# Kernel tuning notes

Measured on AMD Instinct MI355X. Metric: run time of the kernel, lower is better.

## Reference

```python
import jax, jax.numpy as jnp
import numpy as np

D_MODEL, NHEAD, D_K = 512, 8, 64
MIN_RBF, MAX_RBF = 0.1, 0.9
MIN_SPREAD, MAX_SPREAD, BASE = 1.0, 6.0, 20.0
LN_EPS = 1e-5


def _layernorm(x, w, b):
    mu = jnp.mean(x, axis=-1, keepdims=True)
    var = jnp.var(x, axis=-1, keepdims=True)
    return (x - mu) * jax.lax.rsqrt(var + LN_EPS) * w + b


def setup_inputs() -> dict:
    key = jax.random.key(0)
    ks = jax.random.split(key, 10)
    B, N = 1, 2048
    inp = {
        "q": jax.random.normal(ks[0], (B, N, D_MODEL), jnp.float32),
        "k": jax.random.normal(ks[1], (B, N, D_MODEL), jnp.float32),
        "v": jax.random.normal(ks[2], (B, N, D_MODEL), jnp.float32),
        "coords": jax.random.normal(ks[3], (B, N, 3), jnp.float32) * 3.0,
        "key_padding_mask": jnp.zeros((B, N), bool),
        # learned params (torch.randn init for projections, LN defaults)
        "q_proj": jax.random.normal(ks[4], (NHEAD, D_MODEL, D_K), jnp.float32),
        "k_proj": jax.random.normal(ks[5], (NHEAD, D_MODEL, D_K), jnp.float32),
        "v_proj": jax.random.normal(ks[6], (NHEAD, D_MODEL, D_K), jnp.float32),
        "q_ln_w": jnp.ones((D_K,), jnp.float32), "q_ln_b": jnp.zeros((D_K,), jnp.float32),
        "k_ln_w": jnp.ones((D_K,), jnp.float32), "k_ln_b": jnp.zeros((D_K,), jnp.float32),
        "v_ln_w": jnp.ones((D_K,), jnp.float32), "v_ln_b": jnp.zeros((D_K,), jnp.float32),
        "out_w": jax.random.normal(ks[7], (D_MODEL, D_MODEL), jnp.float32) / np.sqrt(D_MODEL),
        "out_b": jnp.zeros((D_MODEL,), jnp.float32),
    }
    return inp


def reference(q, k, v, coords, key_padding_mask,
              q_proj, k_proj, v_proj,
              q_ln_w, q_ln_b, k_ln_w, k_ln_b, v_ln_w, v_ln_b,
              out_w, out_b):
    B, N, _ = q.shape
    # per-head projections: [B,H,N,dk]
    Q = _layernorm(jnp.einsum('bnd,hdk->bhnk', q, q_proj), q_ln_w, q_ln_b)
    K = _layernorm(jnp.einsum('bnd,hdk->bhnk', k, k_proj), k_ln_w, k_ln_b)
    V = _layernorm(jnp.einsum('bnd,hdk->bhnk', v, v_proj), v_ln_w, v_ln_b)

    # head-specific gaussian spreads (torch.logspace(0,1,H,base) semantics)
    spreads = MIN_SPREAD + (MAX_SPREAD - MIN_SPREAD) * (BASE ** jnp.linspace(0.0, 1.0, NHEAD) - 1.0) / (BASE - 1.0)

    # pairwise squared distances [B,N,N] -> per-head RBF [B,H,N,N]
    d2 = jnp.sum((coords[:, :, None, :] - coords[:, None, :, :]) ** 2, axis=-1)
    rbf = jnp.exp(-d2[:, None, :, :] / (2.0 * spreads[None, :, None, None] ** 2))
    rbf = jnp.clip(rbf, MIN_RBF, MAX_RBF)

    # RBF-modulated scaled dot-product attention
    scores = jnp.einsum('bhik,bhjk->bhij', Q, K) / np.sqrt(D_K) * rbf
    scores = jnp.where(key_padding_mask[:, None, None, :], -1e9, scores)
    P = jax.nn.softmax(scores, axis=-1)
    out = jnp.einsum('bhij,bhjk->bhik', P, V)  # [B,H,N,dk]

    # torch: out.permute(0,2,3,1).reshape(B,N,d_model)
    out = jnp.transpose(out, (0, 2, 3, 1)).reshape(B, N, D_MODEL)
    return out @ out_w.T + out_b
```

## Files before the change

kernel.cpp:

```cpp
#include <hip/hip_runtime.h>
#include <math.h>

#define N_TOK 2048
#define D_MODEL 512
#define NHEAD 8
#define DK 64
#define LOG2E 1.44269504f
#define QSCALE 0.18033688f
#define KTILE 6144
#define KHEAD (32 * KTILE)

typedef __attribute__((ext_vector_type(8))) short short8;
typedef __attribute__((ext_vector_type(4))) short short4v;
typedef __attribute__((ext_vector_type(4))) float f32x4;

__device__ __forceinline__ short f2bf(float x) {
    unsigned u = __float_as_uint(x);
    u = (u + 0x7fffu + ((u >> 16) & 1u)) >> 16;
    return (short)u;
}

__device__ __forceinline__ float bf2f(short s) {
    return __uint_as_float(((unsigned)(unsigned short)s) << 16);
}

__device__ __forceinline__ void split2(float x, short& h_, short& l_) {
    h_ = f2bf(x);
    l_ = f2bf(x - bf2f(h_));
}

__device__ __forceinline__ void split3(float x, short& h_, short& m_, short& l_) {
    h_ = f2bf(x);
    float r = x - bf2f(h_);
    m_ = f2bf(r);
    l_ = f2bf(r - bf2f(m_));
}

__device__ __forceinline__ unsigned cvt_pk_bf16(float lo, float hi) {
    unsigned r;
    asm("v_cvt_pk_bf16_f32 %0, %1, %2" : "=v"(r) : "v"(lo), "v"(hi));
    return r;
}

__device__ __forceinline__ float head_c(int h) {
    float tt = (float)h * (1.0f / 7.0f);
    float sp = 1.0f + 5.0f * (__builtin_exp2f(tt * 4.3219281f) - 1.0f) * (1.0f / 19.0f);
    return -LOG2E / (2.0f * sp * sp);
}

__global__ __launch_bounds__(256) void prep_all_kernel(
    const float* __restrict__ q, const float* __restrict__ k,
    const float* __restrict__ v, const float* __restrict__ coords,
    const unsigned char* __restrict__ mask,
    const float* __restrict__ qp, const float* __restrict__ kp,
    const float* __restrict__ vp, const float* __restrict__ ow,
    short* __restrict__ Xbf, short* __restrict__ Wt, short* __restrict__ Wo,
    short* __restrict__ Kf, float* __restrict__ mpen,
    unsigned* __restrict__ tflag)
{
    __shared__ float tile[64][65];
    const int bid = blockIdx.x;
    const int t = threadIdx.x;

    if (bid < 1536) {
        int i = bid * 256 + t;
        int tt = i >> 17;
        int rem = i & 131071;
        const float4* src = (const float4*)(tt == 0 ? q : (tt == 1 ? k : v));
        float4 a = src[rem * 2], b = src[rem * 2 + 1];
        short8 o;
        o[0] = f2bf(a.x); o[1] = f2bf(a.y); o[2] = f2bf(a.z); o[3] = f2bf(a.w);
        o[4] = f2bf(b.x); o[5] = f2bf(b.y); o[6] = f2bf(b.z); o[7] = f2bf(b.w);
        *(short8*)(Xbf + (size_t)i * 8) = o;
    } else if (bid < 1792) {
        int i = bid - 1536;
        int z = i >> 6;
        int bx = i & 7, by = (i >> 3) & 7;
        if (z == 3) {
            int m0 = bx * 64, j0 = by * 64, hh = by;
            for (int ii = t; ii < 4096; ii += 256) {
                int r = ii >> 6, kk = ii & 63;
                Wo[(size_t)(m0 + r) * 512 + j0 + kk] =
                    f2bf(ow[(size_t)(m0 + r) * 512 + kk * 8 + hh]);
            }
            return;
        }
        const float* src = z == 0 ? qp : (z == 1 ? kp : vp);
        const int h = bx, d0 = by * 64;
        for (int ii = t; ii < 4096; ii += 256) {
            int r = ii >> 6, c = ii & 63;
            tile[r][c] = src[((size_t)h * 512 + d0 + r) * 64 + c];
        }
        __syncthreads();
        short* W = Wt + (size_t)z * 512 * 512;
        for (int ii = t; ii < 4096; ii += 256) {
            int cr = ii >> 6, dc_ = ii & 63;
            W[(size_t)(h * 64 + cr) * 512 + d0 + dc_] = f2bf(tile[dc_][cr]);
        }
    } else {
        int j = (bid - 1792) * 256 + t;
        float x = coords[j * 3 + 0], y = coords[j * 3 + 1], z = coords[j * 3 + 2];
        unsigned char mk = mask[j];
        mpen[j] = mk ? -1e9f : 0.f;
        unsigned long long b = __ballot(mk != 0);
        if ((t & 63) == 0) tflag[j >> 6] = (b != 0ull) ? 1u : 0u;
        float n2 = x * x + y * y + z * z;
        const short one = (short)0x3F80;
        const int kr = j & 15;
        #pragma unroll
        for (int h = 0; h < NHEAD; ++h) {
            float c = head_c(h);
            short ahx, alx, ahy, aly, ahz, alz, k2a, k2b, k2c;
            split2(-2.f * c * x, ahx, alx);
            split2(-2.f * c * y, ahy, aly);
            split2(-2.f * c * z, ahz, alz);
            split3(c * n2, k2a, k2b, k2c);
            short8 g0, g1, g2;
            g0[0] = ahx; g0[1] = alx; g0[2] = ahx; g0[3] = ahy;
            g0[4] = aly; g0[5] = ahy; g0[6] = ahz; g0[7] = alz;
            g1[0] = ahz; g1[1] = alx; g1[2] = aly; g1[3] = alz;
            g1[4] = k2a; g1[5] = k2b; g1[6] = k2c; g1[7] = one;
            g2[0] = one; g2[1] = one;
            #pragma unroll
            for (int e = 2; e < 8; ++e) g2[e] = 0;
            short8 g3;
            #pragma unroll
            for (int e = 0; e < 8; ++e) g3[e] = 0;
            short* base = Kf + (size_t)h * KHEAD + (size_t)(j >> 6) * KTILE
                        + 4096 + (size_t)((j >> 4) & 3) * 512;
            *(short8*)(base + (size_t)(0 * 16 + kr) * 8) = g0;
            *(short8*)(base + (size_t)(1 * 16 + kr) * 8) = g1;
            *(short8*)(base + (size_t)(2 * 16 + kr) * 8) = g2;
            *(short8*)(base + (size_t)(3 * 16 + kr) * 8) = g3;
        }
    }
}

__global__ __launch_bounds__(256) void proj_ln_mfma_kernel(
    const short* __restrict__ Xbf, const short* __restrict__ Wt,
    const float* __restrict__ qlw, const float* __restrict__ qlb,
    const float* __restrict__ klw, const float* __restrict__ klb,
    const float* __restrict__ vlw, const float* __restrict__ vlb,
    short* __restrict__ Qbf, short* __restrict__ Kf, short* __restrict__ Vf)
{
    __shared__ short Xs[64 * 64];
    __shared__ short Ws[64 * 64];
    const int z = blockIdx.z, h = blockIdx.y;
    const int n0 = blockIdx.x * 64;
    const int tid = threadIdx.x, w = tid >> 6, l = tid & 63;
    const int l15 = l & 15, lg = l >> 4;

    const short* X = Xbf + (size_t)z * N_TOK * D_MODEL;
    const short* Wz = Wt + ((size_t)z * 512 + h * 64) * 512;

    const f32x4 zero4 = {0.f, 0.f, 0.f, 0.f};
    f32x4 acc[4];
    #pragma unroll
    for (int dc = 0; dc < 4; ++dc) acc[dc] = zero4;

    for (int kb = 0; kb < 8; ++kb) {
        const int d0 = kb * 64;
        __syncthreads();
        #pragma unroll
        for (int i = 0; i < 2; ++i) {
            int c = tid + i * 256;
            int r = c >> 3, g = c & 7;
            short8 xv = *(const short8*)(X + (size_t)(n0 + r) * 512 + d0 + g * 8);
            *(short8*)(Xs + r * 64 + ((g * 8) ^ ((r & 7) << 3))) = xv;
            short8 wv = *(const short8*)(Wz + (size_t)r * 512 + d0 + g * 8);
            *(short8*)(Ws + r * 64 + ((g * 8) ^ ((r & 7) << 3))) = wv;
        }
        __syncthreads();
        const int arow = w * 16 + l15;
        short8 a0 = *(const short8*)(Xs + arow * 64 + ((lg * 8) ^ ((arow & 7) << 3)));
        short8 a1 = *(const short8*)(Xs + arow * 64 + ((32 + lg * 8) ^ ((arow & 7) << 3)));
        #pragma unroll
        for (int dc = 0; dc < 4; ++dc) {
            const int brow = dc * 16 + l15;
            short8 b0 = *(const short8*)(Ws + brow * 64 + ((lg * 8) ^ ((brow & 7) << 3)));
            acc[dc] = __builtin_amdgcn_mfma_f32_16x16x32_bf16(a0, b0, acc[dc], 0, 0, 0);
            short8 b1 = *(const short8*)(Ws + brow * 64 + ((32 + lg * 8) ^ ((brow & 7) << 3)));
            acc[dc] = __builtin_amdgcn_mfma_f32_16x16x32_bf16(a1, b1, acc[dc], 0, 0, 0);
        }
    }

    const float* lw  = z == 0 ? qlw : (z == 1 ? klw : vlw);
    const float* lbp = z == 0 ? qlb : (z == 1 ? klb : vlb);
    float wv_[4], bv_[4];
    #pragma unroll
    for (int dc = 0; dc < 4; ++dc) {
        wv_[dc] = lw[dc * 16 + l15];
        bv_[dc] = lbp[dc * 16 + l15];
    }
    float mu[4], rs[4];
    #pragma unroll
    for (int reg = 0; reg < 4; ++reg) {
        float s = acc[0][reg] + acc[1][reg] + acc[2][reg] + acc[3][reg];
        #pragma unroll
        for (int off = 1; off < 16; off <<= 1) s += __shfl_xor(s, off);
        float m = s * (1.0f / 64.0f);
        float ss = 0.f;
        #pragma unroll
        for (int dc = 0; dc < 4; ++dc) { float d = acc[dc][reg] - m; ss += d * d; }
        #pragma unroll
        for (int off = 1; off < 16; off <<= 1) ss += __shfl_xor(ss, off);
        mu[reg] = m;
        rs[reg] = rsqrtf(ss * (1.0f / 64.0f) + 1e-5f);
    }

    const int tile = n0 >> 6;
    if (z == 0) {
        #pragma unroll
        for (int dc = 0; dc < 4; ++dc)
            #pragma unroll
            for (int reg = 0; reg < 4; ++reg) {
                int n = n0 + w * 16 + lg * 4 + reg;
                float val = ((acc[dc][reg] - mu[reg]) * rs[reg] * wv_[dc] + bv_[dc]) * QSCALE;
                Qbf[((size_t)h * N_TOK + n) * DK + dc * 16 + l15] = f2bf(val);
            }
    } else if (z == 1) {
        short* Kh = Kf + (size_t)h * KHEAD;
        #pragma unroll
        for (int dc = 0; dc < 4; ++dc) {
            int hf  = dc >> 1;
            int lgc = ((dc & 1) << 1) | (l15 >> 3);
            int e   = l15 & 7;
            size_t base = (size_t)tile * KTILE + (w * 2 + hf) * 512 + 16 * 8 * lgc + e;
            #pragma unroll
            for (int reg = 0; reg < 4; ++reg) {
                float val = (acc[dc][reg] - mu[reg]) * rs[reg] * wv_[dc] + bv_[dc];
                Kh[base + (lg * 4 + reg) * 8] = f2bf(val);
            }
        }
    } else {
        short* Vh = Vf + (size_t)h * N_TOK * DK;
        int hfv = w >> 1;
        int lgv = ((w & 1) << 1) | (lg >> 1);
        int eb  = (lg & 1) * 4;
        #pragma unroll
        for (int dc = 0; dc < 4; ++dc) {
            short4v p;
            #pragma unroll
            for (int reg = 0; reg < 4; ++reg)
                p[reg] = f2bf((acc[dc][reg] - mu[reg]) * rs[reg] * wv_[dc] + bv_[dc]);
            size_t addr = (size_t)tile * 4096 + (dc * 2 + hfv) * 512 + (l15 + 16 * lgv) * 8 + eb;
            *(short4v*)(Vh + addr) = p;
        }
    }
}

__global__ __launch_bounds__(256) void attn_kernel(
    const short* __restrict__ Qbf, const short* __restrict__ Kf,
    const short* __restrict__ Vf, const float* __restrict__ coords,
    const float* __restrict__ mpen, const unsigned* __restrict__ tflag,
    short* __restrict__ PO, float* __restrict__ PL)
{
    __shared__ short Pls[4][1024];
    __shared__ float bufO[2][64][17];
    __shared__ float bufL[2][64];

    const int tid = threadIdx.x;
    const int w = tid >> 6, l = tid & 63;
    const int l15 = l & 15, lg = l >> 4;
    const int bid = blockIdx.x;
    const int h  = bid & 7;
    const int nt = (bid >> 3) & 127;
    const int z  = bid >> 10;
    const int n0 = nt * 16;

    char* Pb = (char*)&Pls[w][0];
    const int psw = (l15 & 7) << 4;

    const short* Qrow = Qbf + ((size_t)h * N_TOK + n0 + l15) * DK + lg * 8;
    const short8 qf0 = *(const short8*)(Qrow);
    const short8 qf1 = *(const short8*)(Qrow + 32);

    const float ch = head_c(h);
    const float qx = coords[(n0 + l15) * 3 + 0];
    const float qy = coords[(n0 + l15) * 3 + 1];
    const float qz = coords[(n0 + l15) * 3 + 2];
    const float cq2 = ch * (qx * qx + qy * qy + qz * qz);
    short8 qaug;
    {
        const short one = (short)0x3F80;
        short qhx, qlx, qhy, qly, qhz, qlz, q2a, q2b, q2c;
        split2(qx, qhx, qlx);
        split2(qy, qhy, qly);
        split2(qz, qhz, qlz);
        split3(cq2, q2a, q2b, q2c);
        #pragma unroll
        for (int e = 0; e < 8; ++e) qaug[e] = 0;
        if (lg == 0) {
            qaug[0] = qhx; qaug[1] = qhx; qaug[2] = qlx; qaug[3] = qhy;
            qaug[4] = qhy; qaug[5] = qly; qaug[6] = qhz; qaug[7] = qhz;
        } else if (lg == 1) {
            qaug[0] = qlz; qaug[1] = qlx; qaug[2] = qly; qaug[3] = qlz;
            qaug[4] = one; qaug[5] = one; qaug[6] = one; qaug[7] = q2a;
        } else if (lg == 2) {
            qaug[0] = q2b; qaug[1] = q2c;
        }
    }

    short8 ones8;
    #pragma unroll
    for (int i = 0; i < 8; ++i) ones8[i] = (short)0x3F80;

    const f32x4 zero4 = {0.f, 0.f, 0.f, 0.f};
    f32x4 oacc[4];
    f32x4 oacc_l = zero4;
    #pragma unroll
    for (int i = 0; i < 4; ++i) oacc[i] = zero4;

    const short* Kfh = Kf + (size_t)h * KHEAD;
    const short* Vfh = Vf + (size_t)h * N_TOK * DK;

    for (int t = 0; t < 4; ++t) {
        const int kt = (z * 4 + w) * 4 + t;
        const int kbase = kt * 64;
        const short* kp = Kfh + (size_t)kt * KTILE + l * 8;
        const short* ap = Kfh + (size_t)kt * KTILE + 4096 + l * 8;
        const short* vp = Vfh + (size_t)kt * 4096 + l * 8;

        f32x4 sacc[4], aacc[4];
        #pragma unroll
        for (int nc = 0; nc < 4; ++nc) {
            short8 k0 = *(const short8*)(kp + nc * 1024);
            short8 k1 = *(const short8*)(kp + nc * 1024 + 512);
            short8 ka = *(const short8*)(ap + nc * 512);
            sacc[nc] = __builtin_amdgcn_mfma_f32_16x16x32_bf16(k0, qf0, zero4, 0, 0, 0);
            sacc[nc] = __builtin_amdgcn_mfma_f32_16x16x32_bf16(k1, qf1, sacc[nc], 0, 0, 0);
            aacc[nc] = __builtin_amdgcn_mfma_f32_16x16x32_bf16(ka, qaug, zero4, 0, 0, 0);
        }

        #pragma unroll
        for (int nc = 0; nc < 4; ++nc) {
            #pragma unroll
            for (int reg = 0; reg < 4; ++reg) {
                float rb = __builtin_exp2f(aacc[nc][reg]);
                rb = fminf(fmaxf(rb, 0.1f), 0.9f);
                sacc[nc][reg] *= rb;
            }
        }
        if (tflag[kt]) {
            #pragma unroll
            for (int nc = 0; nc < 4; ++nc)
                #pragma unroll
                for (int reg = 0; reg < 4; ++reg)
                    sacc[nc][reg] += mpen[kbase + nc * 16 + lg * 4 + reg];
        }

        #pragma unroll
        for (int nc = 0; nc < 4; ++nc) {
            float p0 = __builtin_exp2f(sacc[nc][0]);
            float p1 = __builtin_exp2f(sacc[nc][1]);
            float p2 = __builtin_exp2f(sacc[nc][2]);
            float p3 = __builtin_exp2f(sacc[nc][3]);
            uint2 u;
            u.x = cvt_pk_bf16(p0, p1);
            u.y = cvt_pk_bf16(p2, p3);
            *(uint2*)(Pb + ((l15 * 128 + nc * 32 + lg * 8) ^ psw)) = u;
        }

        short8 pf0 = *(const short8*)(Pb + ((l15 * 128 + lg * 16) ^ psw));
        short8 pf1 = *(const short8*)(Pb + ((l15 * 128 + 64 + lg * 16) ^ psw));
        #pragma unroll
        for (int dcc = 0; dcc < 4; ++dcc) {
            short8 v0 = *(const short8*)(vp + dcc * 1024);
            short8 v1 = *(const short8*)(vp + dcc * 1024 + 512);
            oacc[dcc] = __builtin_amdgcn_mfma_f32_16x16x32_bf16(v0, pf0, oacc[dcc], 0, 0, 0);
            oacc[dcc] = __builtin_amdgcn_mfma_f32_16x16x32_bf16(v1, pf1, oacc[dcc], 0, 0, 0);
        }
        oacc_l = __builtin_amdgcn_mfma_f32_16x16x32_bf16(ones8, pf0, oacc_l, 0, 0, 0);
        oacc_l = __builtin_amdgcn_mfma_f32_16x16x32_bf16(ones8, pf1, oacc_l, 0, 0, 0);
    }

    float l_ = oacc_l[0];

    if (w >= 2) {
        int slot = w - 2;
        bufL[slot][l] = l_;
        #pragma unroll
        for (int dc = 0; dc < 4; ++dc)
            #pragma unroll
            for (int reg = 0; reg < 4; ++reg)
                bufO[slot][l][dc * 4 + reg] = oacc[dc][reg];
    }
    __syncthreads();
    if (w < 2) {
        l_ += bufL[w][l];
        #pragma unroll
        for (int dc = 0; dc < 4; ++dc)
            #pragma unroll
            for (int reg = 0; reg < 4; ++reg)
                oacc[dc][reg] += bufO[w][l][dc * 4 + reg];
    }
    __syncthreads();
    if (w == 1) {
        bufL[0][l] = l_;
        #pragma unroll
        for (int dc = 0; dc < 4; ++dc)
            #pragma unroll
            for (int reg = 0; reg < 4; ++reg)
                bufO[0][l][dc * 4 + reg] = oacc[dc][reg];
    }
    __syncthreads();
    if (w == 0) {
        float lf = l_ + bufL[0][l];
        size_t p = ((size_t)z * NHEAD + h) * N_TOK + n0 + l15;
        if (lg == 0) PL[p] = lf;
        #pragma unroll
        for (int dcc = 0; dcc < 4; ++dcc) {
            short4v o4;
            #pragma unroll
            for (int reg = 0; reg < 4; ++reg)
                o4[reg] = f2bf(oacc[dcc][reg] + bufO[0][l][dcc * 4 + reg]);
            *(short4v*)(PO + p * 64 + dcc * 16 + lg * 4) = o4;
        }
    }
}

__global__ __launch_bounds__(256) void out_proj_kernel(
    const short* __restrict__ PO, const float* __restrict__ PL,
    const short* __restrict__ Wo, const float* __restrict__ bias,
    float* __restrict__ out)
{
    __shared__ short As[64 * 64];
    __shared__ short Bs[64 * 64];
    const int n0 = blockIdx.x * 64, m0 = blockIdx.y * 64;
    const int tid = threadIdx.x, w = tid >> 6, l = tid & 63;
    const int l15 = l & 15, lg = l >> 4;

    const f32x4 zero4 = {0.f, 0.f, 0.f, 0.f};
    f32x4 acc[4];
    #pragma unroll
    for (int dc = 0; dc < 4; ++dc) acc[dc] = zero4;

    for (int kb = 0; kb < 8; ++kb) {
        const int j0 = kb * 64;
        __syncthreads();
        #pragma unroll
        for (int i = 0; i < 2; ++i) {
            int c = tid + i * 256;
            int r = c >> 3, g = c & 7;
            int n = n0 + r;
            size_t p0 = (size_t)kb * N_TOK + n;
            size_t p1 = (size_t)(NHEAD + kb) * N_TOK + n;
            float rl = 1.0f / (PL[p0] + PL[p1]);
            short8 a0 = *(const short8*)(PO + p0 * 64 + g * 8);
            short8 a1 = *(const short8*)(PO + p1 * 64 + g * 8);
            short8 av;
            #pragma unroll
            for (int e = 0; e < 8; ++e)
                av[e] = f2bf((bf2f(a0[e]) + bf2f(a1[e])) * rl);
            *(short8*)(As + r * 64 + ((g * 8) ^ ((r & 7) << 3))) = av;
            short8 bv = *(const short8*)(Wo + (size_t)(m0 + r) * 512 + j0 + g * 8);
            *(short8*)(Bs + r * 64 + ((g * 8) ^ ((r & 7) << 3))) = bv;
        }
        __syncthreads();
        const int arow = w * 16 + l15;
        short8 a0 = *(const short8*)(As + arow * 64 + ((lg * 8) ^ ((arow & 7) << 3)));
        short8 a1 = *(const short8*)(As + arow * 64 + ((32 + lg * 8) ^ ((arow & 7) << 3)));
        #pragma unroll
        for (int dc = 0; dc < 4; ++dc) {
            const int brow = dc * 16 + l15;
            short8 b0 = *(const short8*)(Bs + brow * 64 + ((lg * 8) ^ ((brow & 7) << 3)));
            acc[dc] = __builtin_amdgcn_mfma_f32_16x16x32_bf16(a0, b0, acc[dc], 0, 0, 0);
            short8 b1 = *(const short8*)(Bs + brow * 64 + ((32 + lg * 8) ^ ((brow & 7) << 3)));
            acc[dc] = __builtin_amdgcn_mfma_f32_16x16x32_bf16(a1, b1, acc[dc], 0, 0, 0);
        }
    }

    #pragma unroll
    for (int dc = 0; dc < 4; ++dc) {
        float bm = bias[m0 + dc * 16 + l15];
        #pragma unroll
        for (int reg = 0; reg < 4; ++reg) {
            int n = n0 + w * 16 + lg * 4 + reg;
            out[(size_t)n * D_MODEL + m0 + dc * 16 + l15] = acc[dc][reg] + bm;
        }
    }
}

extern "C" void kernel_launch(void* const* d_in, const int* in_sizes, int n_in,
                              void* d_out, int out_size, void* d_ws, size_t ws_size,
                              hipStream_t stream)
{
    const float* q      = (const float*)d_in[0];
    const float* k      = (const float*)d_in[1];
    const float* v      = (const float*)d_in[2];
    const float* coords = (const float*)d_in[3];
    const unsigned char* mask = (const unsigned char*)d_in[4];
    const float* q_proj = (const float*)d_in[5];
    const float* k_proj = (const float*)d_in[6];
    const float* v_proj = (const float*)d_in[7];
    const float* q_ln_w = (const float*)d_in[8];
    const float* q_ln_b = (const float*)d_in[9];
    const float* k_ln_w = (const float*)d_in[10];
    const float* k_ln_b = (const float*)d_in[11];
    const float* v_ln_w = (const float*)d_in[12];
    const float* v_ln_b = (const float*)d_in[13];
    const float* out_w  = (const float*)d_in[14];
    const float* out_b  = (const float*)d_in[15];
    float* out = (float*)d_out;

    short* Xbf = (short*)d_ws;
    short* Wt  = Xbf + 3145728;
    short* Wo  = Wt + 786432;
    short* Qbf = Wo + 262144;
    short* Kf  = Qbf + 1048576;
    short* Vf  = Kf + 1572864;
    float* mpen = (float*)(Vf + 1048576);
    unsigned* tflag = (unsigned*)(mpen + 2048);

    short* PO = Xbf;
    float* PL = (float*)Wt;

    prep_all_kernel<<<dim3(1800), dim3(256), 0, stream>>>(
        q, k, v, coords, mask, q_proj, k_proj, v_proj, out_w,
        Xbf, Wt, Wo, Kf, mpen, tflag);
    proj_ln_mfma_kernel<<<dim3(32, 8, 3), dim3(256), 0, stream>>>(
        Xbf, Wt, q_ln_w, q_ln_b, k_ln_w, k_ln_b, v_ln_w, v_ln_b, Qbf, Kf, Vf);
    attn_kernel<<<dim3(2048), dim3(256), 0, stream>>>(
        Qbf, Kf, Vf, coords, mpen, tflag, PO, PL);
    out_proj_kernel<<<dim3(32, 8), dim3(256), 0, stream>>>(PO, PL, Wo, out_b, out);
}
```

Baseline: 66.85 us.

## Process two 16-query tiles per attention block to reuse K/V fragment loads

Each attention block now handles 32 query rows (two 16-row halves) instead of 16, so each K, augmented-coordinate and V fragment loaded from global memory feeds twice as many MFMAs. The grid is halved to 1024 blocks and the LDS staging and cross-wave reduction buffers are doubled to match. This cuts global/L2 traffic for K and V per query but doubles accumulator registers per thread, which may lower occupancy. A launch-bounds hint of three blocks per CU is added.

Measured after the change: 68.29 us. 2.1% more time.

```diff
diff --git a/kernel.cpp b/kernel.cpp
--- a/kernel.cpp
+++ b/kernel.cpp
@@ -249,67 +249,75 @@
     }
 }
 
-__global__ __launch_bounds__(256) void attn_kernel(
+__global__ __launch_bounds__(256, 3) void attn_kernel(
     const short* __restrict__ Qbf, const short* __restrict__ Kf,
     const short* __restrict__ Vf, const float* __restrict__ coords,
     const float* __restrict__ mpen, const unsigned* __restrict__ tflag,
     short* __restrict__ PO, float* __restrict__ PL)
 {
-    __shared__ short Pls[4][1024];
-    __shared__ float bufO[2][64][17];
-    __shared__ float bufL[2][64];
+    __shared__ short Pls[4][2048];
+    __shared__ float bufO[2][64][33];
+    __shared__ float bufL[2][64][2];
 
     const int tid = threadIdx.x;
     const int w = tid >> 6, l = tid & 63;
     const int l15 = l & 15, lg = l >> 4;
     const int bid = blockIdx.x;
     const int h  = bid & 7;
-    const int nt = (bid >> 3) & 127;
-    const int z  = bid >> 10;
-    const int n0 = nt * 16;
-
-    char* Pb = (char*)&Pls[w][0];
+    const int nt = (bid >> 3) & 63;
+    const int z  = bid >> 9;
+    const int n0 = nt * 32;
+
+    char* PbA = (char*)&Pls[w][0];
+    char* PbB = (char*)&Pls[w][1024];
     const int psw = (l15 & 7) << 4;
 
-    const short* Qrow = Qbf + ((size_t)h * N_TOK + n0 + l15) * DK + lg * 8;
-    const short8 qf0 = *(const short8*)(Qrow);
-    const short8 qf1 = *(const short8*)(Qrow + 32);
+    const short* QrowA = Qbf + ((size_t)h * N_TOK + n0 + l15) * DK + lg * 8;
+    const short8 qfA0 = *(const short8*)(QrowA);
+    const short8 qfA1 = *(const short8*)(QrowA + 32);
+    const short* QrowB = QrowA + 16 * DK;
+    const short8 qfB0 = *(const short8*)(QrowB);
+    const short8 qfB1 = *(const short8*)(QrowB + 32);
 
     const float ch = head_c(h);
-    const float qx = coords[(n0 + l15) * 3 + 0];
-    const float qy = coords[(n0 + l15) * 3 + 1];
-    const float qz = coords[(n0 + l15) * 3 + 2];
-    const float cq2 = ch * (qx * qx + qy * qy + qz * qz);
-    short8 qaug;
-    {
-        const short one = (short)0x3F80;
+    const short one = (short)0x3F80;
+    short8 qaugA, qaugB;
+    #pragma unroll
+    for (int half = 0; half < 2; ++half) {
+        int n = n0 + half * 16 + l15;
+        float qx = coords[n * 3 + 0];
+        float qy = coords[n * 3 + 1];
+        float qz = coords[n * 3 + 2];
+        float cq2 = ch * (qx * qx + qy * qy + qz * qz);
         short qhx, qlx, qhy, qly, qhz, qlz, q2a, q2b, q2c;
         split2(qx, qhx, qlx);
         split2(qy, qhy, qly);
         split2(qz, qhz, qlz);
         split3(cq2, q2a, q2b, q2c);
-        #pragma unroll
-        for (int e = 0; e < 8; ++e) qaug[e] = 0;
+        short8 qa;
+        #pragma unroll
+        for (int e = 0; e < 8; ++e) qa[e] = 0;
         if (lg == 0) {
-            qaug[0] = qhx; qaug[1] = qhx; qaug[2] = qlx; qaug[3] = qhy;
-            qaug[4] = qhy; qaug[5] = qly; qaug[6] = qhz; qaug[7] = qhz;
+            qa[0] = qhx; qa[1] = qhx; qa[2] = qlx; qa[3] = qhy;
+            qa[4] = qhy; qa[5] = qly; qa[6] = qhz; qa[7] = qhz;
         } else if (lg == 1) {
-            qaug[0] = qlz; qaug[1] = qlx; qaug[2] = qly; qaug[3] = qlz;
-            qaug[4] = one; qaug[5] = one; qaug[6] = one; qaug[7] = q2a;
+            qa[0] = qlz; qa[1] = qlx; qa[2] = qly; qa[3] = qlz;
+            qa[4] = one; qa[5] = one; qa[6] = one; qa[7] = q2a;
         } else if (lg == 2) {
-            qaug[0] = q2b; qaug[1] = q2c;
-        }
+            qa[0] = q2b; qa[1] = q2c;
+        }
+        if (half == 0) qaugA = qa; else qaugB = qa;
     }
 
     short8 ones8;
     #pragma unroll
-    for (int i = 0; i < 8; ++i) ones8[i] = (short)0x3F80;
+    for (int i = 0; i < 8; ++i) ones8[i] = one;
 
     const f32x4 zero4 = {0.f, 0.f, 0.f, 0.f};
-    f32x4 oacc[4];
-    f32x4 oacc_l = zero4;
-    #pragma unroll
-    for (int i = 0; i < 4; ++i) oacc[i] = zero4;
+    f32x4 oaccA[4], oaccB[4];
+    f32x4 olA = zero4, olB = zero4;
+    #pragma unroll
+    for (int i = 0; i < 4; ++i) { oaccA[i] = zero4; oaccB[i] = zero4; }
 
     const short* Kfh = Kf + (size_t)h * KHEAD;
     const short* Vfh = Vf + (size_t)h * N_TOK * DK;
@@ -318,103 +326,131 @@
         const int kt = (z * 4 + w) * 4 + t;
         const int kbase = kt * 64;
         const short* kp = Kfh + (size_t)kt * KTILE + l * 8;
-        const short* ap = Kfh + (size_t)kt * KTILE + 4096 + l * 8;
+        const short* ap = kp + 4096;
         const short* vp = Vfh + (size_t)kt * 4096 + l * 8;
 
-        f32x4 sacc[4], aacc[4];
+        f32x4 sA[4], sB[4], aA[4], aB[4];
         #pragma unroll
         for (int nc = 0; nc < 4; ++nc) {
             short8 k0 = *(const short8*)(kp + nc * 1024);
             short8 k1 = *(const short8*)(kp + nc * 1024 + 512);
             short8 ka = *(const short8*)(ap + nc * 512);
-            sacc[nc] = __builtin_amdgcn_mfma_f32_16x16x32_bf16(k0, qf0, zero4, 0, 0, 0);
-            sacc[nc] = __builtin_amdgcn_mfma_f32_16x16x32_bf16(k1, qf1, sacc[nc], 0, 0, 0);
-            aacc[nc] = __builtin_amdgcn_mfma_f32_16x16x32_bf16(ka, qaug, zero4, 0, 0, 0);
+            sA[nc] = __builtin_amdgcn_mfma_f32_16x16x32_bf16(k0, qfA0, zero4, 0, 0, 0);
+            sA[nc] = __builtin_amdgcn_mfma_f32_16x16x32_bf16(k1, qfA1, sA[nc], 0, 0, 0);
+            sB[nc] = __builtin_amdgcn_mfma_f32_16x16x32_bf16(k0, qfB0, zero4, 0, 0, 0);
+            sB[nc] = __builtin_amdgcn_mfma_f32_16x16x32_bf16(k1, qfB1, sB[nc], 0, 0, 0);
+            aA[nc] = __builtin_amdgcn_mfma_f32_16x16x32_bf16(ka, qaugA, zero4, 0, 0, 0);
+            aB[nc] = __builtin_amdgcn_mfma_f32_16x16x32_bf16(ka, qaugB, zero4, 0, 0, 0);
         }
 
         #pragma unroll
         for (int nc = 0; nc < 4; ++nc) {
             #pragma unroll
             for (int reg = 0; reg < 4; ++reg) {
-                float rb = __builtin_exp2f(aacc[nc][reg]);
-                rb = fminf(fmaxf(rb, 0.1f), 0.9f);
-                sacc[nc][reg] *= rb;
+                float rbA = __builtin_exp2f(aA[nc][reg]);
+                rbA = fminf(fmaxf(rbA, 0.1f), 0.9f);
+                sA[nc][reg] *= rbA;
+                float rbB = __builtin_exp2f(aB[nc][reg]);
+                rbB = fminf(fmaxf(rbB, 0.1f), 0.9f);
+                sB[nc][reg] *= rbB;
             }
         }
         if (tflag[kt]) {
             #pragma unroll
             for (int nc = 0; nc < 4; ++nc)
                 #pragma unroll
-                for (int reg = 0; reg < 4; ++reg)
-                    sacc[nc][reg] += mpen[kbase + nc * 16 + lg * 4 + reg];
+                for (int reg = 0; reg < 4; ++reg) {
+                    float mp = mpen[kbase + nc * 16 + lg * 4 + reg];
+                    sA[nc][reg] += mp;
+                    sB[nc][reg] += mp;
+                }
         }
 
         #pragma unroll
         for (int nc = 0; nc < 4; ++nc) {
-            float p0 = __builtin_exp2f(sacc[nc][0]);
-            float p1 = __builtin_exp2f(sacc[nc][1]);
-            float p2 = __builtin_exp2f(sacc[nc][2]);
-            float p3 = __builtin_exp2f(sacc[nc][3]);
-            uint2 u;
-            u.x = cvt_pk_bf16(p0, p1);
-            u.y = cvt_pk_bf16(p2, p3);
-            *(uint2*)(Pb + ((l15 * 128 + nc * 32 + lg * 8) ^ psw)) = u;
-        }
-
-        short8 pf0 = *(const short8*)(Pb + ((l15 * 128 + lg * 16) ^ psw));
-        short8 pf1 = *(const short8*)(Pb + ((l15 * 128 + 64 + lg * 16) ^ psw));
+            uint2 uA, uB;
+            uA.x = cvt_pk_bf16(__builtin_exp2f(sA[nc][0]), __builtin_exp2f(sA[nc][1]));
+            uA.y = cvt_pk_bf16(__builtin_exp2f(sA[nc][2]), __builtin_exp2f(sA[nc][3]));
+            uB.x = cvt_pk_bf16(__builtin_exp2f(sB[nc][0]), __builtin_exp2f(sB[nc][1]));
+            uB.y = cvt_pk_bf16(__builtin_exp2f(sB[nc][2]), __builtin_exp2f(sB[nc][3]));
+            *(uint2*)(PbA + ((l15 * 128 + nc * 32 + lg * 8) ^ psw)) = uA;
+            *(uint2*)(PbB + ((l15 * 128 + nc * 32 + lg * 8) ^ psw)) = uB;
+        }
+
+        short8 pfA0 = *(const short8*)(PbA + ((l15 * 128 + lg * 16) ^ psw));
+        short8 pfA1 = *(const short8*)(PbA + ((l15 * 128 + 64 + lg * 16) ^ psw));
+        short8 pfB0 = *(const short8*)(PbB + ((l15 * 128 + lg * 16) ^ psw));
+        short8 pfB1 = *(const short8*)(PbB + ((l15 * 128 + 64 + lg * 16) ^ psw));
         #pragma unroll
         for (int dcc = 0; dcc < 4; ++dcc) {
             short8 v0 = *(const short8*)(vp + dcc * 1024);
             short8 v1 = *(const short8*)(vp + dcc * 1024 + 512);
-            oacc[dcc] = __builtin_amdgcn_mfma_f32_16x16x32_bf16(v0, pf0, oacc[dcc], 0, 0, 0);
-            oacc[dcc] = __builtin_amdgcn_mfma_f32_16x16x32_bf16(v1, pf1, oacc[dcc], 0, 0, 0);
-        }
-        oacc_l = __builtin_amdgcn_mfma_f32_16x16x32_bf16(ones8, pf0, oacc_l, 0, 0, 0);
-        oacc_l = __builtin_amdgcn_mfma_f32_16x16x32_bf16(ones8, pf1, oacc_l, 0, 0, 0);
-    }
-
-    float l_ = oacc_l[0];
+            oaccA[dcc] = __builtin_amdgcn_mfma_f32_16x16x32_bf16(v0, pfA0, oaccA[dcc], 0, 0, 0);
+            oaccA[dcc] = __builtin_amdgcn_mfma_f32_16x16x32_bf16(v1, pfA1, oaccA[dcc], 0, 0, 0);
+            oaccB[dcc] = __builtin_amdgcn_mfma_f32_16x16x32_bf16(v0, pfB0, oaccB[dcc], 0, 0, 0);
+            oaccB[dcc] = __builtin_amdgcn_mfma_f32_16x16x32_bf16(v1, pfB1, oaccB[dcc], 0, 0, 0);
+        }
+        olA = __builtin_amdgcn_mfma_f32_16x16x32_bf16(ones8, pfA0, olA, 0, 0, 0);
+        olA = __builtin_amdgcn_mfma_f32_16x16x32_bf16(ones8, pfA1, olA, 0, 0, 0);
+        olB = __builtin_amdgcn_mfma_f32_16x16x32_bf16(ones8, pfB0, olB, 0, 0, 0);
+        olB = __builtin_amdgcn_mfma_f32_16x16x32_bf16(ones8, pfB1, olB, 0, 0, 0);
+    }
+
+    float lA = olA[0], lB = olB[0];
 
     if (w >= 2) {
         int slot = w - 2;
-        bufL[slot][l] = l_;
+        bufL[slot][l][0] = lA;
+        bufL[slot][l][1] = lB;
         #pragma unroll
         for (int dc = 0; dc < 4; ++dc)
             #pragma unroll
-            for (int reg = 0; reg < 4; ++reg)
-                bufO[slot][l][dc * 4 + reg] = oacc[dc][reg];
+            for (int reg = 0; reg < 4; ++reg) {
+                bufO[slot][l][dc * 4 + reg] = oaccA[dc][reg];
+                bufO[slot][l][16 + dc * 4 + reg] = oaccB[dc][reg];
+            }
     }
     __syncthreads();
     if (w < 2) {
-        l_ += bufL[w][l];
+        lA += bufL[w][l][0];
+        lB += bufL[w][l][1];
         #pragma unroll
         for (int dc = 0; dc < 4; ++dc)
             #pragma unroll
-            for (int reg = 0; reg < 4; ++reg)
-                oacc[dc][reg] += bufO[w][l][dc * 4 + reg];
+            for (int reg = 0; reg < 4; ++reg) {
+                oaccA[dc][reg] += bufO[w][l][dc * 4 + reg];
+                oaccB[dc][reg] += bufO[w][l][16 + dc * 4 + reg];
+            }
     }
     __syncthreads();
     if (w == 1) {
-        bufL[0][l] = l_;
+        bufL[0][l][0] = lA;
+        bufL[0][l][1] = lB;
         #pragma unroll
         for (int dc = 0; dc < 4; ++dc)
             #pragma unroll
-            for (int reg = 0; reg < 4; ++reg)
-                bufO[0][l][dc * 4 + reg] = oacc[dc][reg];
+            for (int reg = 0; reg < 4; ++reg) {
+                bufO[0][l][dc * 4 + reg] = oaccA[dc][reg];
+                bufO[0][l][16 + dc * 4 + reg] = oaccB[dc][reg];
+            }
     }
     __syncthreads();
     if (w == 0) {
-        float lf = l_ + bufL[0][l];
-        size_t p = ((size_t)z * NHEAD + h) * N_TOK + n0 + l15;
-        if (lg == 0) PL[p] = lf;
+        float lfA = lA + bufL[0][l][0];
+        float lfB = lB + bufL[0][l][1];
+        size_t pA = ((size_t)z * NHEAD + h) * N_TOK + n0 + l15;
+        size_t pB = pA + 16;
+        if (lg == 0) { PL[pA] = lfA; PL[pB] = lfB; }
         #pragma unroll
         for (int dcc = 0; dcc < 4; ++dcc) {
-            short4v o4;
-            #pragma unroll
-            for (int reg = 0; reg < 4; ++reg)
-                o4[reg] = f2bf(oacc[dcc][reg] + bufO[0][l][dcc * 4 + reg]);
-            *(short4v*)(PO + p * 64 + dcc * 16 + lg * 4) = o4;
+            short4v oA, oB;
+            #pragma unroll
+            for (int reg = 0; reg < 4; ++reg) {
+                oA[reg] = f2bf(oaccA[dcc][reg] + bufO[0][l][dcc * 4 + reg]);
+                oB[reg] = f2bf(oaccB[dcc][reg] + bufO[0][l][16 + dcc * 4 + reg]);
+            }
+            *(short4v*)(PO + pA * 64 + dcc * 16 + lg * 4) = oA;
+            *(short4v*)(PO + pB * 64 + dcc * 16 + lg * 4) = oB;
         }
     }
 }
@@ -520,7 +556,7 @@
         Xbf, Wt, Wo, Kf, mpen, tflag);
     proj_ln_mfma_kernel<<<dim3(32, 8, 3), dim3(256), 0, stream>>>(
         Xbf, Wt, q_ln_w, q_ln_b, k_ln_w, k_ln_b, v_ln_w, v_ln_b, Qbf, Kf, Vf);
-    attn_kernel<<<dim3(2048), dim3(256), 0, stream>>>(
+    attn_kernel<<<dim3(1024), dim3(256), 0, stream>>>(
         Qbf, Kf, Vf, coords, mpen, tflag, PO, PL);
     out_proj_kernel<<<dim3(32, 8), dim3(256), 0, stream>>>(PO, PL, Wo, out_b, out);
 }
```

## Fuse fp32-to-bf16 input conversion into projection GEMM and double row tile

Applied to the files above, without the earlier changes.

Drops the separate pass in the prep kernel that wrote bf16 copies of q/k/v. The projection kernel now reads fp32 inputs directly and converts them while staging into shared memory. Each block also covers 128 tokens instead of 64, so every loaded weight tile feeds twice as many MFMAs and the grid shrinks to 384 blocks. The workspace layout is reshuffled to match. The trade-off is that each projection block reads twice the bytes per input element (fp32) and has fewer blocks to spread across CUs.

Result: no change. 67.88 us (+1.5%).

```diff
diff --git a/kernel.cpp b/kernel.cpp
--- a/kernel.cpp
+++ b/kernel.cpp
@@ -49,12 +49,10 @@
 }
 
 __global__ __launch_bounds__(256) void prep_all_kernel(
-    const float* __restrict__ q, const float* __restrict__ k,
-    const float* __restrict__ v, const float* __restrict__ coords,
-    const unsigned char* __restrict__ mask,
+    const float* __restrict__ coords, const unsigned char* __restrict__ mask,
     const float* __restrict__ qp, const float* __restrict__ kp,
     const float* __restrict__ vp, const float* __restrict__ ow,
-    short* __restrict__ Xbf, short* __restrict__ Wt, short* __restrict__ Wo,
+    short* __restrict__ Wt, short* __restrict__ Wo,
     short* __restrict__ Kf, float* __restrict__ mpen,
     unsigned* __restrict__ tflag)
 {
@@ -62,18 +60,8 @@
     const int bid = blockIdx.x;
     const int t = threadIdx.x;
 
-    if (bid < 1536) {
-        int i = bid * 256 + t;
-        int tt = i >> 17;
-        int rem = i & 131071;
-        const float4* src = (const float4*)(tt == 0 ? q : (tt == 1 ? k : v));
-        float4 a = src[rem * 2], b = src[rem * 2 + 1];
-        short8 o;
-        o[0] = f2bf(a.x); o[1] = f2bf(a.y); o[2] = f2bf(a.z); o[3] = f2bf(a.w);
-        o[4] = f2bf(b.x); o[5] = f2bf(b.y); o[6] = f2bf(b.z); o[7] = f2bf(b.w);
-        *(short8*)(Xbf + (size_t)i * 8) = o;
-    } else if (bid < 1792) {
-        int i = bid - 1536;
+    if (bid < 256) {
+        int i = bid;
         int z = i >> 6;
         int bx = i & 7, by = (i >> 3) & 7;
         if (z == 3) {
@@ -98,7 +86,7 @@
             W[(size_t)(h * 64 + cr) * 512 + d0 + dc_] = f2bf(tile[dc_][cr]);
         }
     } else {
-        int j = (bid - 1792) * 256 + t;
+        int j = (bid - 256) * 256 + t;
         float x = coords[j * 3 + 0], y = coords[j * 3 + 1], z = coords[j * 3 + 2];
         unsigned char mk = mask[j];
         mpen[j] = mk ? -1e9f : 0.f;
@@ -137,50 +125,68 @@
 }
 
 __global__ __launch_bounds__(256) void proj_ln_mfma_kernel(
-    const short* __restrict__ Xbf, const short* __restrict__ Wt,
+    const float* __restrict__ xq, const float* __restrict__ xk,
+    const float* __restrict__ xv, const short* __restrict__ Wt,
     const float* __restrict__ qlw, const float* __restrict__ qlb,
     const float* __restrict__ klw, const float* __restrict__ klb,
     const float* __restrict__ vlw, const float* __restrict__ vlb,
     short* __restrict__ Qbf, short* __restrict__ Kf, short* __restrict__ Vf)
 {
-    __shared__ short Xs[64 * 64];
+    __shared__ short Xs[128 * 64];
     __shared__ short Ws[64 * 64];
     const int z = blockIdx.z, h = blockIdx.y;
-    const int n0 = blockIdx.x * 64;
+    const int n0 = blockIdx.x * 128;
     const int tid = threadIdx.x, w = tid >> 6, l = tid & 63;
     const int l15 = l & 15, lg = l >> 4;
 
-    const short* X = Xbf + (size_t)z * N_TOK * D_MODEL;
+    const float* X = z == 0 ? xq : (z == 1 ? xk : xv);
     const short* Wz = Wt + ((size_t)z * 512 + h * 64) * 512;
 
     const f32x4 zero4 = {0.f, 0.f, 0.f, 0.f};
-    f32x4 acc[4];
-    #pragma unroll
-    for (int dc = 0; dc < 4; ++dc) acc[dc] = zero4;
+    f32x4 acc[2][4];
+    #pragma unroll
+    for (int H = 0; H < 2; ++H)
+        #pragma unroll
+        for (int dc = 0; dc < 4; ++dc) acc[H][dc] = zero4;
 
     for (int kb = 0; kb < 8; ++kb) {
         const int d0 = kb * 64;
         __syncthreads();
         #pragma unroll
+        for (int i = 0; i < 8; ++i) {
+            int idx = tid + i * 256;
+            int r = idx >> 4;
+            int f = idx & 15;
+            float4 xv4 = *(const float4*)(X + (size_t)(n0 + r) * 512 + d0 + f * 4);
+            short4v pk;
+            pk[0] = f2bf(xv4.x); pk[1] = f2bf(xv4.y);
+            pk[2] = f2bf(xv4.z); pk[3] = f2bf(xv4.w);
+            *(short4v*)(Xs + r * 64 + (((f >> 1) * 8) ^ ((r & 7) << 3)) + (f & 1) * 4) = pk;
+        }
+        #pragma unroll
         for (int i = 0; i < 2; ++i) {
             int c = tid + i * 256;
             int r = c >> 3, g = c & 7;
-            short8 xv = *(const short8*)(X + (size_t)(n0 + r) * 512 + d0 + g * 8);
-            *(short8*)(Xs + r * 64 + ((g * 8) ^ ((r & 7) << 3))) = xv;
             short8 wv = *(const short8*)(Wz + (size_t)r * 512 + d0 + g * 8);
             *(short8*)(Ws + r * 64 + ((g * 8) ^ ((r & 7) << 3))) = wv;
         }
         __syncthreads();
-        const int arow = w * 16 + l15;
-        short8 a0 = *(const short8*)(Xs + arow * 64 + ((lg * 8) ^ ((arow & 7) << 3)));
-        short8 a1 = *(const short8*)(Xs + arow * 64 + ((32 + lg * 8) ^ ((arow & 7) << 3)));
+        const int arowA = w * 16 + l15;
+        const int arowB = 64 + arowA;
+        const int asw = (arowA & 7) << 3;
+        short8 aA0 = *(const short8*)(Xs + arowA * 64 + ((lg * 8) ^ asw));
+        short8 aA1 = *(const short8*)(Xs + arowA * 64 + ((32 + lg * 8) ^ asw));
+        short8 aB0 = *(const short8*)(Xs + arowB * 64 + ((lg * 8) ^ asw));
+        short8 aB1 = *(const short8*)(Xs + arowB * 64 + ((32 + lg * 8) ^ asw));
         #pragma unroll
         for (int dc = 0; dc < 4; ++dc) {
             const int brow = dc * 16 + l15;
             short8 b0 = *(const short8*)(Ws + brow * 64 + ((lg * 8) ^ ((brow & 7) << 3)));
-            acc[dc] = __builtin_amdgcn_mfma_f32_16x16x32_bf16(a0, b0, acc[dc], 0, 0, 0);
             short8 b1 = *(const short8*)(Ws + brow * 64 + ((32 + lg * 8) ^ ((brow & 7) << 3)));
-            acc[dc] = __builtin_amdgcn_mfma_f32_16x16x32_bf16(a1, b1, acc[dc], 0, 0, 0);
+            acc[0][dc] = __builtin_amdgcn_mfma_f32_16x16x32_bf16(aA0, b0, acc[0][dc], 0, 0, 0);
+            acc[0][dc] = __builtin_amdgcn_mfma_f32_16x16x32_bf16(aA1, b1, acc[0][dc], 0, 0, 0);
+            acc[1][dc] = __builtin_amdgcn_mfma_f32_16x16x32_bf16(aB0, b0, acc[1][dc], 0, 0, 0);
+            acc[1][dc] = __builtin_amdgcn_mfma_f32_16x16x32_bf16(aB1, b1, acc[1][dc], 0, 0, 0);
         }
     }
 
@@ -192,59 +198,63 @@
         wv_[dc] = lw[dc * 16 + l15];
         bv_[dc] = lbp[dc * 16 + l15];
     }
-    float mu[4], rs[4];
-    #pragma unroll
-    for (int reg = 0; reg < 4; ++reg) {
-        float s = acc[0][reg] + acc[1][reg] + acc[2][reg] + acc[3][reg];
-        #pragma unroll
-        for (int off = 1; off < 16; off <<= 1) s += __shfl_xor(s, off);
-        float m = s * (1.0f / 64.0f);
-        float ss = 0.f;
-        #pragma unroll
-        for (int dc = 0; dc < 4; ++dc) { float d = acc[dc][reg] - m; ss += d * d; }
-        #pragma unroll
-        for (int off = 1; off < 16; off <<= 1) ss += __shfl_xor(ss, off);
-        mu[reg] = m;
-        rs[reg] = rsqrtf(ss * (1.0f / 64.0f) + 1e-5f);
-    }
-
-    const int tile = n0 >> 6;
-    if (z == 0) {
-        #pragma unroll
-        for (int dc = 0; dc < 4; ++dc)
-            #pragma unroll
-            for (int reg = 0; reg < 4; ++reg) {
-                int n = n0 + w * 16 + lg * 4 + reg;
-                float val = ((acc[dc][reg] - mu[reg]) * rs[reg] * wv_[dc] + bv_[dc]) * QSCALE;
-                Qbf[((size_t)h * N_TOK + n) * DK + dc * 16 + l15] = f2bf(val);
+
+    #pragma unroll
+    for (int H = 0; H < 2; ++H) {
+        const int nb = n0 + H * 64;
+        const int tile = nb >> 6;
+        float mu[4], rs[4];
+        #pragma unroll
+        for (int reg = 0; reg < 4; ++reg) {
+            float s = acc[H][0][reg] + acc[H][1][reg] + acc[H][2][reg] + acc[H][3][reg];
+            #pragma unroll
+            for (int off = 1; off < 16; off <<= 1) s += __shfl_xor(s, off);
+            float m = s * (1.0f / 64.0f);
+            float ss = 0.f;
+            #pragma unroll
+            for (int dc = 0; dc < 4; ++dc) { float d = acc[H][dc][reg] - m; ss += d * d; }
+            #pragma unroll
+            for (int off = 1; off < 16; off <<= 1) ss += __shfl_xor(ss, off);
+            mu[reg] = m;
+            rs[reg] = rsqrtf(ss * (1.0f / 64.0f) + 1e-5f);
+        }
+        if (z == 0) {
+            #pragma unroll
+            for (int dc = 0; dc < 4; ++dc)
+                #pragma unroll
+                for (int reg = 0; reg < 4; ++reg) {
+                    int n = nb + w * 16 + lg * 4 + reg;
+                    float val = ((acc[H][dc][reg] - mu[reg]) * rs[reg] * wv_[dc] + bv_[dc]) * QSCALE;
+                    Qbf[((size_t)h * N_TOK + n) * DK + dc * 16 + l15] = f2bf(val);
+                }
+        } else if (z == 1) {
+            short* Kh = Kf + (size_t)h * KHEAD;
+            #pragma unroll
+            for (int dc = 0; dc < 4; ++dc) {
+                int hf  = dc >> 1;
+                int lgc = ((dc & 1) << 1) | (l15 >> 3);
+                int e   = l15 & 7;
+                size_t base = (size_t)tile * KTILE + (w * 2 + hf) * 512 + 16 * 8 * lgc + e;
+                #pragma unroll
+                for (int reg = 0; reg < 4; ++reg) {
+                    float val = (acc[H][dc][reg] - mu[reg]) * rs[reg] * wv_[dc] + bv_[dc];
+                    Kh[base + (lg * 4 + reg) * 8] = f2bf(val);
+                }
             }
-    } else if (z == 1) {
-        short* Kh = Kf + (size_t)h * KHEAD;
-        #pragma unroll
-        for (int dc = 0; dc < 4; ++dc) {
-            int hf  = dc >> 1;
-            int lgc = ((dc & 1) << 1) | (l15 >> 3);
-            int e   = l15 & 7;
-            size_t base = (size_t)tile * KTILE + (w * 2 + hf) * 512 + 16 * 8 * lgc + e;
-            #pragma unroll
-            for (int reg = 0; reg < 4; ++reg) {
-                float val = (acc[dc][reg] - mu[reg]) * rs[reg] * wv_[dc] + bv_[dc];
-                Kh[base + (lg * 4 + reg) * 8] = f2bf(val);
+        } else {
+            short* Vh = Vf + (size_t)h * N_TOK * DK;
+            int hfv = w >> 1;
+            int lgv = ((w & 1) << 1) | (lg >> 1);
+            int eb  = (lg & 1) * 4;
+            #pragma unroll
+            for (int dc = 0; dc < 4; ++dc) {
+                short4v p;
+                #pragma unroll
+                for (int reg = 0; reg < 4; ++reg)
+                    p[reg] = f2bf((acc[H][dc][reg] - mu[reg]) * rs[reg] * wv_[dc] + bv_[dc]);
+                size_t addr = (size_t)tile * 4096 + (dc * 2 + hfv) * 512 + (l15 + 16 * lgv) * 8 + eb;
+                *(short4v*)(Vh + addr) = p;
             }
-        }
-    } else {
-        short* Vh = Vf + (size_t)h * N_TOK * DK;
-        int hfv = w >> 1;
-        int lgv = ((w & 1) << 1) | (lg >> 1);
-        int eb  = (lg & 1) * 4;
-        #pragma unroll
-        for (int dc = 0; dc < 4; ++dc) {
-            short4v p;
-            #pragma unroll
-            for (int reg = 0; reg < 4; ++reg)
-                p[reg] = f2bf((acc[dc][reg] - mu[reg]) * rs[reg] * wv_[dc] + bv_[dc]);
-            size_t addr = (size_t)tile * 4096 + (dc * 2 + hfv) * 512 + (l15 + 16 * lgv) * 8 + eb;
-            *(short4v*)(Vh + addr) = p;
         }
     }
 }
@@ -318,7 +328,7 @@
         const int kt = (z * 4 + w) * 4 + t;
         const int kbase = kt * 64;
         const short* kp = Kfh + (size_t)kt * KTILE + l * 8;
-        const short* ap = Kfh + (size_t)kt * KTILE + 4096 + l * 8;
+        const short* ap = kp + 4096;
         const short* vp = Vfh + (size_t)kt * 4096 + l * 8;
 
         f32x4 sacc[4], aacc[4];
@@ -503,23 +513,20 @@
     const float* out_b  = (const float*)d_in[15];
     float* out = (float*)d_out;
 
-    short* Xbf = (short*)d_ws;
-    short* Wt  = Xbf + 3145728;
+    short* PO  = (short*)d_ws;
+    short* Wt  = PO + 2097152;
     short* Wo  = Wt + 786432;
     short* Qbf = Wo + 262144;
     short* Kf  = Qbf + 1048576;
     short* Vf  = Kf + 1572864;
     float* mpen = (float*)(Vf + 1048576);
     unsigned* tflag = (unsigned*)(mpen + 2048);
-
-    short* PO = Xbf;
-    float* PL = (float*)Wt;
-
-    prep_all_kernel<<<dim3(1800), dim3(256), 0, stream>>>(
-        q, k, v, coords, mask, q_proj, k_proj, v_proj, out_w,
-        Xbf, Wt, Wo, Kf, mpen, tflag);
-    proj_ln_mfma_kernel<<<dim3(32, 8, 3), dim3(256), 0, stream>>>(
-        Xbf, Wt, q_ln_w, q_ln_b, k_ln_w, k_ln_b, v_ln_w, v_ln_b, Qbf, Kf, Vf);
+    float* PL = (float*)(tflag + 32);
+
+    prep_all_kernel<<<dim3(264), dim3(256), 0, stream>>>(
+        coords, mask, q_proj, k_proj, v_proj, out_w, Wt, Wo, Kf, mpen, tflag);
+    proj_ln_mfma_kernel<<<dim3(16, 8, 3), dim3(256), 0, stream>>>(
+        q, k, v, Wt, q_ln_w, q_ln_b, k_ln_w, k_ln_b, v_ln_w, v_ln_b, Qbf, Kf, Vf);
     attn_kernel<<<dim3(2048), dim3(256), 0, stream>>>(
         Qbf, Kf, Vf, coords, mpen, tflag, PO, PL);
     out_proj_kernel<<<dim3(32, 8), dim3(256), 0, stream>>>(PO, PL, Wo, out_b, out);
```
